# Performance work log

Measured on AMD Instinct MI355X. Metric: run time of the kernel, lower is better.

The kernel has to match this reference:

```python
import jax, jax.numpy as jnp
import numpy as np

B, DIM, DIMH, DIMC = 1024, 32, 1024, 512
SQRT_HALF_PI = float(np.sqrt(np.pi / 2.0))
SQRT2 = float(np.sqrt(2.0))


def _gsp(x):
    """gaussian_softplus activation from ConditionalICNN."""
    return (SQRT_HALF_PI * x * jax.scipy.special.erf(x / SQRT2)
            + jnp.exp(-0.5 * x * x) + SQRT_HALF_PI * x) / (2.0 * SQRT_HALF_PI)


def setup_inputs() -> dict:
    key = jax.random.key(0)
    _i = [0]
    def nrm(shape, s=0.05):
        _i[0] += 1
        return jax.random.normal(jax.random.fold_in(key, _i[0]), shape, dtype=jnp.float32) * s
    inp = {
        "x": nrm((B, DIM), 1.0),
        "c": nrm((B, DIMC), 1.0),
        # w0 init: log(exp(1)-1) as in DeepConvexFlow
        "w0": jnp.full((1,), float(np.log(np.e - 1.0)), dtype=jnp.float32),
        "w1": jnp.zeros((1,), dtype=jnp.float32),
        "Wz0_w": nrm((DIMH, DIM)), "Wz0_b": nrm((DIMH,)),
        "Wc0_w": nrm((DIMH, DIMC)), "Wc0_b": nrm((DIMH,)),
        "an0_b": nrm((DIMH,)), "an0_logs": nrm((DIMH,), 0.01),
        "Wz1_w": nrm((DIMH, DIMH)), "Wz1_b": nrm((DIMH,)),
        "Wx1_w": nrm((DIMH, DIM)), "Wx1_b": nrm((DIMH,)),
        "Wc1_w": nrm((DIMH, DIMC)), "Wc1_b": nrm((DIMH,)),
        "an1_b": nrm((DIMH,)), "an1_logs": nrm((DIMH,), 0.01),
        "Wz2_w": nrm((DIMH, DIMH)), "Wz2_b": nrm((DIMH,)),
        "Wx2_w": nrm((DIMH, DIM)), "Wx2_b": nrm((DIMH,)),
        "Wc2_w": nrm((DIMH, DIMC)), "Wc2_b": nrm((DIMH,)),
        "an2_b": nrm((DIMH,)), "an2_logs": nrm((DIMH,), 0.01),
        "Wzout_w": nrm((1, DIMH)), "Wxout_w": nrm((1, DIM)), "Wcout_w": nrm((1, DIMC)),
    }
    return inp


def reference(x, c, w0, w1,
              Wz0_w, Wz0_b, Wc0_w, Wc0_b, an0_b, an0_logs,
              Wz1_w, Wz1_b, Wx1_w, Wx1_b, Wc1_w, Wc1_b, an1_b, an1_logs,
              Wz2_w, Wz2_b, Wx2_w, Wx2_b, Wc2_w, Wc2_b, an2_b, an2_logs,
              Wzout_w, Wxout_w, Wcout_w):
    """ConditionalDeepConvexFlow.forward_transform with exact logdet.
    Returns (f = grad_x F(x), logdet = logabsdet of per-sample Hessian)."""

    def pot(x1, c1):  # scalar convex potential F for one sample
        h = Wz0_w @ x1 + Wz0_b + Wc0_w @ c1 + Wc0_b
        z = _gsp((h + an0_b) * jnp.exp(an0_logs))  # ActNormNoLogdet + act
        for (Wz_w, Wz_b, Wx_w, Wx_b, Wc_w, Wc_b, an_b, an_logs) in (
                (Wz1_w, Wz1_b, Wx1_w, Wx1_b, Wc1_w, Wc1_b, an1_b, an1_logs),
                (Wz2_w, Wz2_b, Wx2_w, Wx2_b, Wc2_w, Wc2_b, an2_b, an2_logs)):
            # PosLinear: softplus(W) with gain 1/in_features
            h = (jax.nn.softplus(Wz_w) @ z) / DIMH + Wz_b \
                + Wx_w @ x1 + Wx_b + Wc_w @ c1 + Wc_b
            z = _gsp((h + an_b) * jnp.exp(an_logs))
        icnn = (jax.nn.softplus(Wzout_w) @ z)[0] / DIMH \
               + (Wxout_w @ x1)[0] + (Wcout_w @ c1)[0]
        return jax.nn.softplus(w1)[0] * icnn \
               + jax.nn.softplus(w0)[0] * 0.5 * jnp.sum(x1 * x1)

    f = jax.vmap(jax.grad(pot))(x, c)          # [B, DIM]
    H = jax.vmap(jax.hessian(pot))(x, c)       # [B, DIM, DIM]
    logdet = jnp.linalg.slogdet(H)[1]          # [B]
    return f, logdet
```

## Files before the change

### kernel.cpp

```cpp
#include <hip/hip_runtime.h>

constexpr int NB   = 1024;
constexpr int NDIM = 32;
constexpr int NH   = 1024;
constexpr int NC   = 512;
constexpr int NS   = 8;
constexpr int KSF  = 8;

constexpr float INV_SQRT2PI = 0.3989422804014327f;
constexpr float SQRT_HALF   = 0.70710678118654752f;
constexpr float SQRT_HPI    = 1.2533141373155003f;

typedef __attribute__((ext_vector_type(8))) short short8;
typedef __attribute__((ext_vector_type(4))) short short4v;
typedef __attribute__((ext_vector_type(4))) float float4v;

__device__ __forceinline__ float sp_f(float x) {
  return (x > 20.f) ? x : log1pf(expf(x));
}

__device__ __forceinline__ short f2bf(float f) {
  union { float f; unsigned u; } x; x.f = f;
  const unsigned r = x.u + 0x7fffu + ((x.u >> 16) & 1u);
  return (short)(r >> 16);
}

__device__ __forceinline__ float bf2f(short s) {
  union { unsigned u; float f; } c;
  c.u = ((unsigned)(unsigned short)s) << 16;
  return c.f;
}

__device__ __forceinline__ void async_ld16(const void* g, void* l) {
  __builtin_amdgcn_global_load_lds(
      (const __attribute__((address_space(1))) void*)g,
      (__attribute__((address_space(3))) void*)l, 16, 0, 0);
}

__global__ __launch_bounds__(256) void k_prep(
    const float* __restrict__ Wz1, const float* __restrict__ Wz2,
    const float* __restrict__ Wzout, const float* __restrict__ Wz0,
    const float* __restrict__ Wx1, const float* __restrict__ Wx2,
    const float* __restrict__ Wc0, const float* __restrict__ Wc1,
    const float* __restrict__ Wc2, const float* __restrict__ Cc,
    short* __restrict__ S1b, short* __restrict__ S1Tb,
    short* __restrict__ S2b, short* __restrict__ S2Tb,
    short* __restrict__ Wc0b, short* __restrict__ Wc1b, short* __restrict__ Wc2b,
    short* __restrict__ Ccb, short* __restrict__ W0Tb,
    short* __restrict__ Wx1Tb, short* __restrict__ Wx2Tb,
    float* __restrict__ so)
{
  const int idx = blockIdx.x * 256 + threadIdx.x;
  const int i = idx >> 10, p = idx & 1023;
  const float v1 = sp_f(Wz1[idx]);
  const short b1 = f2bf(v1);
  S1b[idx] = b1; S1Tb[p * NH + i] = b1;
  const float v2 = sp_f(Wz2[idx]);
  const short b2 = f2bf(v2);
  S2b[idx] = b2; S2Tb[p * NH + i] = b2;
  if (idx < NH) so[idx] = sp_f(Wzout[idx]);
  if (idx < NH * NC) {
    Wc0b[idx] = f2bf(Wc0[idx]);
    Wc1b[idx] = f2bf(Wc1[idx]);
    Wc2b[idx] = f2bf(Wc2[idx]);
  }
  if (idx < NB * NC) Ccb[idx] = f2bf(Cc[idx]);
  if (idx < NDIM * NH) {
    const int j = idx >> 10, pp = idx & 1023;
    W0Tb[idx]  = f2bf(Wz0[pp * NDIM + j]);
    Wx1Tb[idx] = f2bf(Wx1[pp * NDIM + j]);
    Wx2Tb[idx] = f2bf(Wx2[pp * NDIM + j]);
  }
}

template<int EPI>
__global__ __launch_bounds__(256) void k_gemm(
    const float* __restrict__ A, const float* __restrict__ Bt,
    float* __restrict__ C, int K, int lda, float scale)
{
  __shared__ float As[16][68];
  __shared__ float Bs[16][68];
  const int tid  = threadIdx.y * 16 + threadIdx.x;
  const int arow = tid >> 2;
  const int acol = (tid & 3) << 2;
  const int m0 = blockIdx.y << 6;
  const int n0 = blockIdx.x << 6;

  float acc[4][4];
#pragma unroll
  for (int i = 0; i < 4; ++i)
#pragma unroll
    for (int j = 0; j < 4; ++j) acc[i][j] = 0.f;

  const int R = m0 + arow;
  for (int k0 = 0; k0 < K; k0 += 16) {
    const float4 av = *reinterpret_cast<const float4*>(&A[(size_t)R * lda + k0 + acol]);
    As[acol + 0][arow] = av.x; As[acol + 1][arow] = av.y;
    As[acol + 2][arow] = av.z; As[acol + 3][arow] = av.w;
    const float4 bv = *reinterpret_cast<const float4*>(&Bt[(size_t)(n0 + arow) * K + k0 + acol]);
    Bs[acol + 0][arow] = bv.x; Bs[acol + 1][arow] = bv.y;
    Bs[acol + 2][arow] = bv.z; Bs[acol + 3][arow] = bv.w;
    __syncthreads();
#pragma unroll
    for (int kk = 0; kk < 16; ++kk) {
      const float4 a  = *reinterpret_cast<const float4*>(&As[kk][threadIdx.y << 2]);
      const float4 bb = *reinterpret_cast<const float4*>(&Bs[kk][threadIdx.x << 2]);
      const float am[4] = {a.x, a.y, a.z, a.w};
      const float bn[4] = {bb.x, bb.y, bb.z, bb.w};
#pragma unroll
      for (int i2 = 0; i2 < 4; ++i2)
#pragma unroll
        for (int j2 = 0; j2 < 4; ++j2)
          acc[i2][j2] = fmaf(am[i2], bn[j2], acc[i2][j2]);
    }
    __syncthreads();
  }
#pragma unroll
  for (int i2 = 0; i2 < 4; ++i2) {
    const int row = m0 + (threadIdx.y << 2) + i2;
    const int col = n0 + (threadIdx.x << 2);
    float* cp = &C[(size_t)row * NH + col];
    float4 o;
    o.x = acc[i2][0] * scale; o.y = acc[i2][1] * scale;
    o.z = acc[i2][2] * scale; o.w = acc[i2][3] * scale;
    if constexpr (EPI == 1) {
      const float4 cur = *reinterpret_cast<const float4*>(cp);
      o.x += cur.x; o.y += cur.y; o.z += cur.z; o.w += cur.w;
    }
    *reinterpret_cast<float4*>(cp) = o;
  }
}

__global__ __launch_bounds__(256) void k_m128(
    const short* __restrict__ A, const short* __restrict__ Bt,
    float* __restrict__ C, float scale, int K, int ldc)
{
  __shared__ short As[128 * 32];
  __shared__ short Bs[128 * 32];
  const int tid  = threadIdx.x;
  const int wave = tid >> 6, lane = tid & 63;
  const int m0 = blockIdx.x << 7, n0 = blockIdx.y << 7;
  const int wm = (wave >> 1) << 6, wn = (wave & 1) << 6;
  const int qd = lane >> 4, md = lane & 15;
  const int sr = lane >> 2;
  const int sc = (lane & 3) << 3;

  float4v acc[4][4];
#pragma unroll
  for (int i = 0; i < 4; ++i)
#pragma unroll
    for (int j = 0; j < 4; ++j) acc[i][j] = (float4v)(0.f);

  for (int k0 = 0; k0 < K; k0 += 32) {
#pragma unroll
    for (int i = 0; i < 2; ++i) {
      const int ch  = wave * 2 + i;
      const int row = ch * 16 + sr;
      async_ld16(&A [(size_t)(m0 + row) * K + k0 + sc], &As[ch * 512]);
      async_ld16(&Bt[(size_t)(n0 + row) * K + k0 + sc], &Bs[ch * 512]);
    }
    __syncthreads();
    short8 af[4], bfr[4];
#pragma unroll
    for (int t = 0; t < 4; ++t) {
      af[t]  = *(const short8*)&As[(wm + t * 16 + md) * 32 + qd * 8];
      bfr[t] = *(const short8*)&Bs[(wn + t * 16 + md) * 32 + qd * 8];
    }
#pragma unroll
    for (int i = 0; i < 4; ++i)
#pragma unroll
      for (int j = 0; j < 4; ++j)
        acc[i][j] = __builtin_amdgcn_mfma_f32_16x16x32_bf16(bfr[j], af[i], acc[i][j], 0, 0, 0);
    __syncthreads();
  }

#pragma unroll
  for (int i = 0; i < 4; ++i) {
    const int rowg = m0 + wm + i * 16 + md;
#pragma unroll
    for (int j = 0; j < 4; ++j) {
      const int colb = n0 + wn + j * 16 + (qd << 2);
      float4 o;
      o.x = acc[i][j][0] * scale; o.y = acc[i][j][1] * scale;
      o.z = acc[i][j][2] * scale; o.w = acc[i][j][3] * scale;
      *reinterpret_cast<float4*>(&C[(size_t)rowg * ldc + colb]) = o;
    }
  }
}

template<int EPI>
__global__ __launch_bounds__(256) void k_mgemm(
    const short* __restrict__ A, const short* __restrict__ Bt,
    short* __restrict__ o1, short* __restrict__ o2,
    const float* __restrict__ gvec, const float* __restrict__ dvec,
    const short* __restrict__ wepiT,
    float scale, int K, int b0)
{
  __shared__ short As[128 * 32];
  __shared__ short Bs[128 * 32];
  const int tid  = threadIdx.x;
  const int wave = tid >> 6, lane = tid & 63;
  const int m0 = blockIdx.x << 7, n0 = blockIdx.y << 7;
  const int wm = (wave >> 1) << 6, wn = (wave & 1) << 6;
  const int qd = lane >> 4, md = lane & 15;

  float4v acc[4][4];
#pragma unroll
  for (int i = 0; i < 4; ++i)
#pragma unroll
    for (int j = 0; j < 4; ++j) acc[i][j] = (float4v)(0.f);

  const int sr = lane >> 2;
  const int sc = (lane & 3) << 3;

  for (int k0 = 0; k0 < K; k0 += 32) {
#pragma unroll
    for (int i = 0; i < 2; ++i) {
      const int ch  = wave * 2 + i;
      const int row = ch * 16 + sr;
      async_ld16(&A [(size_t)(m0 + row) * K + k0 + sc], &As[ch * 512]);
      async_ld16(&Bt[(size_t)(n0 + row) * K + k0 + sc], &Bs[ch * 512]);
    }
    __syncthreads();
    short8 af[4], bfr[4];
#pragma unroll
    for (int t = 0; t < 4; ++t) {
      af[t]  = *(const short8*)&As[(wm + t * 16 + md) * 32 + qd * 8];
      bfr[t] = *(const short8*)&Bs[(wn + t * 16 + md) * 32 + qd * 8];
    }
#pragma unroll
    for (int i = 0; i < 4; ++i)
#pragma unroll
      for (int j = 0; j < 4; ++j)
        acc[i][j] = __builtin_amdgcn_mfma_f32_16x16x32_bf16(bfr[j], af[i], acc[i][j], 0, 0, 0);
    __syncthreads();
  }

#pragma unroll
  for (int i = 0; i < 4; ++i) {
    const int rowg = m0 + wm + i * 16 + md;
    const int b = b0 + (rowg >> 5);
    const int j2 = rowg & 31;
    const size_t bNH = (size_t)b * NH;
#pragma unroll
    for (int j = 0; j < 4; ++j) {
      const int colb = n0 + wn + j * 16 + (qd << 2);
      const float4 dq = *(const float4*)&dvec[bNH + colb];
      const short4v wq = *(const short4v*)&wepiT[(size_t)j2 * NH + colb];
      const float dqv[4] = {dq.x, dq.y, dq.z, dq.w};
      float v[4];
      short4v o1v;
#pragma unroll
      for (int r = 0; r < 4; ++r) {
        v[r] = acc[i][j][r] * scale + bf2f(wq[r]);
        o1v[r] = f2bf(v[r] * dqv[r]);
      }
      *(short4v*)&o1[(size_t)rowg * NH + colb] = o1v;
      if constexpr (EPI == 2) {
        const float4 gg = *(const float4*)&gvec[bNH + colb];
        const float ggv[4] = {gg.x, gg.y, gg.z, gg.w};
        short4v o2v;
#pragma unroll
        for (int r = 0; r < 4; ++r) o2v[r] = f2bf(v[r] * ggv[r]);
        *(short4v*)&o2[(size_t)rowg * NH + colb] = o2v;
      }
    }
  }
}

__global__ __launch_bounds__(256) void k_mgemm64(
    const short* __restrict__ A, const short* __restrict__ Bt,
    float* __restrict__ C, float scale, int K)
{
  __shared__ short As[64 * 32];
  __shared__ short Bs[64 * 32];
  const int tid  = threadIdx.x;
  const int wave = tid >> 6, lane = tid & 63;
  const int m0 = blockIdx.x << 6, n0 = blockIdx.y << 6;
  const int wm = (wave >> 1) << 5, wn = (wave & 1) << 5;
  const int qd = lane >> 4, md = lane & 15;
  const int sr = lane >> 2;
  const int sc = (lane & 3) << 3;

  float4v acc[2][2];
#pragma unroll
  for (int i = 0; i < 2; ++i)
#pragma unroll
    for (int j = 0; j < 2; ++j) acc[i][j] = (float4v)(0.f);

  for (int k0 = 0; k0 < K; k0 += 32) {
    const int row = wave * 16 + sr;
    async_ld16(&A [(size_t)(m0 + row) * K + k0 + sc], &As[wave * 512]);
    async_ld16(&Bt[(size_t)(n0 + row) * K + k0 + sc], &Bs[wave * 512]);
    __syncthreads();
    short8 af[2], bfr[2];
#pragma unroll
    for (int t = 0; t < 2; ++t) {
      af[t]  = *(const short8*)&As[(wm + t * 16 + md) * 32 + qd * 8];
      bfr[t] = *(const short8*)&Bs[(wn + t * 16 + md) * 32 + qd * 8];
    }
#pragma unroll
    for (int i = 0; i < 2; ++i)
#pragma unroll
      for (int j = 0; j < 2; ++j)
        acc[i][j] = __builtin_amdgcn_mfma_f32_16x16x32_bf16(bfr[j], af[i], acc[i][j], 0, 0, 0);
    __syncthreads();
  }

#pragma unroll
  for (int i = 0; i < 2; ++i) {
    const int rowg = m0 + wm + i * 16 + md;
#pragma unroll
    for (int j = 0; j < 2; ++j) {
      const int colb = n0 + wn + j * 16 + (qd << 2);
      float4 o;
      o.x = acc[i][j][0] * scale; o.y = acc[i][j][1] * scale;
      o.z = acc[i][j][2] * scale; o.w = acc[i][j][3] * scale;
      *reinterpret_cast<float4*>(&C[(size_t)rowg * NH + colb]) = o;
    }
  }
}

__global__ __launch_bounds__(256) void k_act(
    const float* __restrict__ HP, const float* __restrict__ HPC_l,
    const float* __restrict__ bA, const float* __restrict__ bB,
    const float* __restrict__ bC,
    const float* __restrict__ anb, const float* __restrict__ anl,
    short* __restrict__ Zbf, float* __restrict__ G, float* __restrict__ U,
    int hasC)
{
  const int idx = blockIdx.x * 256 + threadIdx.x;
  const int i = idx & 1023;
  float bias = bA[i] + bB[i] + anb[i];
  if (hasC) bias += bC[i];
  const float el = expf(anl[i]);
  const float hc = HPC_l[(size_t)(idx >> 10) * (3 * NH) + i];
  const float a = (HP[idx] + hc + bias) * el;
  const float pdf = expf(-0.5f * a * a);
  const float er = erff(a * SQRT_HALF);
  Zbf[idx] = f2bf((SQRT_HPI * a * er + pdf + SQRT_HPI * a) * INV_SQRT2PI);
  G[idx] = 0.5f * (1.f + er) * el;
  U[idx] = pdf * INV_SQRT2PI * el * el;
}

__global__ __launch_bounds__(256) void k_act2(
    const float* __restrict__ HP, const float* __restrict__ HPC_l,
    const float* __restrict__ bA, const float* __restrict__ bB,
    const float* __restrict__ bC,
    const float* __restrict__ anb, const float* __restrict__ anl,
    const float* __restrict__ so,
    float* __restrict__ SD2, short* __restrict__ D2gbf)
{
  const int idx = blockIdx.x * 256 + threadIdx.x;
  const int i = idx & 1023;
  const float bias = bA[i] + bB[i] + bC[i] + anb[i];
  const float el = expf(anl[i]);
  const float hc = HPC_l[(size_t)(idx >> 10) * (3 * NH) + i];
  const float a = (HP[idx] + hc + bias) * el;
  const float pdf = expf(-0.5f * a * a);
  const float er = erff(a * SQRT_HALF);
  const float g = 0.5f * (1.f + er) * el;
  const float u = pdf * INV_SQRT2PI * el * el;
  const float t2 = so[i] * (1.f / NH);
  SD2[idx] = sqrtf(fmaxf(t2 * u, 0.f));
  D2gbf[idx] = f2bf(t2 * g);
}

__global__ __launch_bounds__(256) void k_bw1(
    const float* __restrict__ T1, const float* __restrict__ G1,
    const float* __restrict__ U1,
    short* __restrict__ E1bf, float* __restrict__ SD1)
{
  const int idx = blockIdx.x * 256 + threadIdx.x;
  const float t = T1[idx];
  E1bf[idx] = f2bf(t * G1[idx]);
  SD1[idx] = sqrtf(fmaxf(t * U1[idx], 0.f));
}

__global__ __launch_bounds__(256) void k_bw0(
    const float* __restrict__ T0, const float* __restrict__ U0,
    const float* __restrict__ G0,
    float* __restrict__ D0, short* __restrict__ GT0b)
{
  const int idx = blockIdx.x * 256 + threadIdx.x;
  const float t = T0[idx];
  D0[idx] = t * U0[idx];
  GT0b[idx] = f2bf(t * G0[idx]);
}

__global__ __launch_bounds__(256) void k_scale0(
    const float* __restrict__ G0, const float* __restrict__ Wz0,
    short* __restrict__ Ah1, int b0)
{
  const int idx = blockIdx.x * 256 + threadIdx.x;
  const int p = idx & 1023, r = idx >> 10;
  const int b = b0 + (r >> 5), j = r & 31;
  Ah1[idx] = f2bf(G0[(size_t)b * NH + p] * Wz0[p * NDIM + j]);
}

__global__ __launch_bounds__(256) void k_fgemm(
    const short* __restrict__ A0, const short* __restrict__ A1,
    const short* __restrict__ A2,
    const short* __restrict__ W0T, const short* __restrict__ W1T,
    const short* __restrict__ W2T,
    float* __restrict__ partF)
{
  const int mb = blockIdx.x;
  const int ks = blockIdx.y;
  const int term = blockIdx.z;
  const short* A  = (term == 0) ? A0 : (term == 1) ? A1 : A2;
  const short* WT = (term == 0) ? W0T : (term == 1) ? W1T : W2T;
  const int wave = threadIdx.x >> 6, lane = threadIdx.x & 63;
  const int qd = lane >> 4, md = lane & 15;
  const int m0 = mb * 128 + wave * 32;
  const int kbeg = ks * (NH / KSF);

  float4v acc[2][2];
#pragma unroll
  for (int i = 0; i < 2; ++i)
#pragma unroll
    for (int j = 0; j < 2; ++j) acc[i][j] = (float4v)(0.f);

  for (int k0 = kbeg; k0 < kbeg + NH / KSF; k0 += 32) {
    const int kk = k0 + qd * 8;
    short8 af[2], bfr[2];
    af[0]  = *(const short8*)&A[(size_t)(m0 + md) * NH + kk];
    af[1]  = *(const short8*)&A[(size_t)(m0 + 16 + md) * NH + kk];
    bfr[0] = *(const short8*)&WT[(size_t)md * NH + kk];
    bfr[1] = *(const short8*)&WT[(size_t)(16 + md) * NH + kk];
#pragma unroll
    for (int i = 0; i < 2; ++i)
#pragma unroll
      for (int j = 0; j < 2; ++j)
        acc[i][j] = __builtin_amdgcn_mfma_f32_16x16x32_bf16(af[i], bfr[j], acc[i][j], 0, 0, 0);
  }

  float* out = &partF[(size_t)(term * KSF + ks) * NB * 32];
#pragma unroll
  for (int i = 0; i < 2; ++i)
#pragma unroll
    for (int j = 0; j < 2; ++j)
#pragma unroll
      for (int r = 0; r < 4; ++r) {
        const int row = m0 + i * 16 + qd * 4 + r;
        const int col = j * 16 + md;
        out[(size_t)row * 32 + col] = acc[i][j][r];
      }
}

__global__ __launch_bounds__(256) void k_fred(
    const float* __restrict__ partF, const float* __restrict__ X,
    const float* __restrict__ Wxout,
    const float* __restrict__ w0p, const float* __restrict__ w1p,
    float* __restrict__ outF)
{
  const int e = blockIdx.x * 256 + threadIdx.x;
  float s = 0.f;
#pragma unroll
  for (int p = 0; p < 3 * KSF; ++p) s += partF[(size_t)p * NB * 32 + e];
  const float spw0 = sp_f(w0p[0]);
  const float spw1 = sp_f(w1p[0]);
  outF[e] = spw1 * (s + Wxout[e & 31]) + spw0 * X[e];
}

__global__ __launch_bounds__(256) void k_gram(
    const short* __restrict__ Q1, const short* __restrict__ Q2,
    const short* __restrict__ W0T, const float* __restrict__ D0,
    float* __restrict__ partH, int b0)
{
  const int ns = blockIdx.x, bl = blockIdx.y;
  const int b = b0 + bl;
  const int wave = threadIdx.x >> 6, lane = threadIdx.x & 63;
  const int wm = (wave >> 1) << 4, wn = (wave & 1) << 4;
  const int qd = lane >> 4, md = lane & 15;
  const int kbeg = ns << 7;
  const size_t rb = (size_t)bl * 32 * NH;

  float4v acc = (float4v)(0.f);

  for (int k0 = kbeg; k0 < kbeg + 128; k0 += 32) {
    const int kk = k0 + qd * 8;
    const short8 ar = *(const short8*)&W0T[(size_t)(wm + md) * NH + kk];
    float dd[8];
    *(float4*)&dd[0] = *(const float4*)&D0[(size_t)b * NH + kk];
    *(float4*)&dd[4] = *(const float4*)&D0[(size_t)b * NH + kk + 4];
    short8 af;
#pragma unroll
    for (int e = 0; e < 8; ++e) af[e] = f2bf(bf2f(ar[e]) * dd[e]);
    const short8 bfr = *(const short8*)&W0T[(size_t)(wn + md) * NH + kk];
    acc = __builtin_amdgcn_mfma_f32_16x16x32_bf16(af, bfr, acc, 0, 0, 0);
  }
#pragma unroll
  for (int l = 0; l < 2; ++l) {
    const short* Q = (l == 0) ? Q1 : Q2;
    for (int k0 = kbeg; k0 < kbeg + 128; k0 += 32) {
      const int kk = k0 + qd * 8;
      const short8 af  = *(const short8*)&Q[rb + (size_t)(wm + md) * NH + kk];
      const short8 bfr = *(const short8*)&Q[rb + (size_t)(wn + md) * NH + kk];
      acc = __builtin_amdgcn_mfma_f32_16x16x32_bf16(af, bfr, acc, 0, 0, 0);
    }
  }

  float* out = &partH[((size_t)bl * NS + ns) * 1024];
#pragma unroll
  for (int r = 0; r < 4; ++r)
    out[(wm + qd * 4 + r) * 32 + (wn + md)] = acc[r];
}

__global__ __launch_bounds__(256) void k_gram2(
    const float* __restrict__ partH,
    const float* __restrict__ w0p, const float* __restrict__ w1p,
    float* __restrict__ outLD, int b0)
{
  const int bl = blockIdx.x, b = b0 + bl, tid = threadIdx.x;
  __shared__ float sH[32][33];
  __shared__ float sred[32];
  const float spw0 = sp_f(w0p[0]);
  const float spw1 = sp_f(w1p[0]);
  const float* base = &partH[(size_t)bl * NS * 1024];
#pragma unroll
  for (int r = 0; r < 4; ++r) {
    const int e = r * 256 + tid;
    float s = 0.f;
#pragma unroll
    for (int ns = 0; ns < NS; ++ns) s += base[ns * 1024 + e];
    float h = s * spw1;
    const int row = e >> 5, col = e & 31;
    if (row == col) h += spw0;
    sH[row][col] = h;
  }
  __syncthreads();

  float ldacc = 0.f;
  for (int c = 0; c < 32; ++c) {
    if (tid >= c && tid < 32) {
      float s = sH[tid][c];
      for (int m = 0; m < c; ++m) s -= sH[tid][m] * sH[c][m];
      sred[tid] = s;
    }
    __syncthreads();
    const float sc = sred[c];
    if (tid >= c && tid < 32) {
      const float lcc = sqrtf(sc);
      sH[tid][c] = (tid == c) ? lcc : sred[tid] / lcc;
    }
    ldacc += logf(sc);
    __syncthreads();
  }
  if (tid == 0) outLD[b] = ldacc;
}

extern "C" void kernel_launch(void* const* d_in, const int* in_sizes, int n_in,
                              void* d_out, int out_size, void* d_ws, size_t ws_size,
                              hipStream_t stream)
{
  const float* X    = (const float*)d_in[0];
  const float* Cc   = (const float*)d_in[1];
  const float* w0   = (const float*)d_in[2];
  const float* w1   = (const float*)d_in[3];
  const float* Wz0w = (const float*)d_in[4];
  const float* Wz0b = (const float*)d_in[5];
  const float* Wc0w = (const float*)d_in[6];
  const float* Wc0b = (const float*)d_in[7];
  const float* an0b = (const float*)d_in[8];
  const float* an0l = (const float*)d_in[9];
  const float* Wz1w = (const float*)d_in[10];
  const float* Wz1b = (const float*)d_in[11];
  const float* Wx1w = (const float*)d_in[12];
  const float* Wx1b = (const float*)d_in[13];
  const float* Wc1w = (const float*)d_in[14];
  const float* Wc1b = (const float*)d_in[15];
  const float* an1b = (const float*)d_in[16];
  const float* an1l = (const float*)d_in[17];
  const float* Wz2w = (const float*)d_in[18];
  const float* Wz2b = (const float*)d_in[19];
  const float* Wx2w = (const float*)d_in[20];
  const float* Wx2b = (const float*)d_in[21];
  const float* Wc2w = (const float*)d_in[22];
  const float* Wc2b = (const float*)d_in[23];
  const float* an2b = (const float*)d_in[24];
  const float* an2l = (const float*)d_in[25];
  const float* Wzoutw = (const float*)d_in[26];
  const float* Wxoutw = (const float*)d_in[27];

  float* ws = (float*)d_ws;
  size_t off = 0;
  auto alloc = [&](size_t n) {
    float* p = ws + off; off += (n + 3) & ~(size_t)3; return p;
  };
  const size_t HH = (size_t)NH * NH;
  const size_t BH = (size_t)NB * NH;

  short* S1b  = (short*)alloc(HH / 2);
  short* S2b  = (short*)alloc(HH / 2);
  short* S1Tb = (short*)alloc(HH / 2);
  short* S2Tb = (short*)alloc(HH / 2);
  short* Wc0bb = (short*)alloc((size_t)NH * NC / 2);
  short* Wc1bb = (short*)alloc((size_t)NH * NC / 2);
  short* Wc2bb = (short*)alloc((size_t)NH * NC / 2);
  short* Ccb  = (short*)alloc((size_t)NB * NC / 2);
  short* W0Tb = (short*)alloc((size_t)NDIM * NH / 2);
  short* Wx1Tb = (short*)alloc((size_t)NDIM * NH / 2);
  short* Wx2Tb = (short*)alloc((size_t)NDIM * NH / 2);
  float* so   = alloc(NH);
  float* HP   = alloc(BH);
  float* HPC  = alloc((size_t)NB * 3 * NH);
  short* Z0b  = (short*)alloc(BH / 2);
  short* Z1b  = (short*)alloc(BH / 2);
  float* G0   = alloc(BH);
  float* U0   = alloc(BH);
  float* G1   = alloc(BH);
  float* U1   = alloc(BH);
  float* SD2  = alloc(BH);
  short* D2gb = (short*)alloc(BH / 2);
  float* T1   = alloc(BH);
  short* E1b  = (short*)alloc(BH / 2);
  float* SD1  = alloc(BH);
  float* T0   = alloc(BH);
  float* D0   = alloc(BH);
  short* GT0b = (short*)alloc(BH / 2);
  float* partF = alloc((size_t)3 * KSF * NB * 32);

  const size_t avail_f = ws_size / sizeof(float);
  int CB = 32;
  const int cands[6] = {1024, 512, 256, 128, 64, 32};
  for (int ci = 0; ci < 6; ++ci) {
    const size_t need = off + 4 * ((size_t)cands[ci] * 32 * NH / 2 + 4)
                      + (size_t)cands[ci] * NS * 1024 + 64;
    if (need <= avail_f) { CB = cands[ci]; break; }
  }
  const size_t chunk_sh = (size_t)CB * 32 * NH;
  short* Ah1 = (short*)alloc(chunk_sh / 2);
  short* A2b = (short*)alloc(chunk_sh / 2);
  short* Q1b = (short*)alloc(chunk_sh / 2);
  short* Q2b = (short*)alloc(chunk_sh / 2);
  float* partH = alloc((size_t)CB * NS * 1024);

  float* outF  = (float*)d_out;
  float* outLD = (float*)d_out + NB * NDIM;

  const dim3 blk2(16, 16);
  const dim3 gridX(16, NB / 64);
  const dim3 gridE(NB * NH / 256);
  const dim3 grid64(NB / 64, NH / 64);
  const dim3 gridC(NB / 128, 3 * NH / 128);
  const float invH = 1.0f / (float)NH;

  k_prep<<<dim3(HH / 256), dim3(256), 0, stream>>>(
      Wz1w, Wz2w, Wzoutw, Wz0w, Wx1w, Wx2w, Wc0w, Wc1w, Wc2w, Cc,
      S1b, S1Tb, S2b, S2Tb, Wc0bb, Wc1bb, Wc2bb, Ccb, W0Tb, Wx1Tb, Wx2Tb, so);

  k_m128<<<gridC, dim3(256), 0, stream>>>(Ccb, Wc0bb, HPC, 1.f, NC, 3 * NH);

  k_gemm<0><<<gridX, blk2, 0, stream>>>(X, Wz0w, HP, NDIM, NDIM, 1.f);
  k_act<<<gridE, dim3(256), 0, stream>>>(HP, HPC + 0 * NH, Wz0b, Wc0b, nullptr,
                                         an0b, an0l, Z0b, G0, U0, 0);
  k_mgemm64<<<grid64, dim3(256), 0, stream>>>(Z0b, S1b, HP, invH, NH);
  k_gemm<1><<<gridX, blk2, 0, stream>>>(X, Wx1w, HP, NDIM, NDIM, 1.f);
  k_act<<<gridE, dim3(256), 0, stream>>>(HP, HPC + 1 * NH, Wz1b, Wx1b, Wc1b,
                                         an1b, an1l, Z1b, G1, U1, 1);
  k_mgemm64<<<grid64, dim3(256), 0, stream>>>(Z1b, S2b, HP, invH, NH);
  k_gemm<1><<<gridX, blk2, 0, stream>>>(X, Wx2w, HP, NDIM, NDIM, 1.f);
  k_act2<<<gridE, dim3(256), 0, stream>>>(HP, HPC + 2 * NH, Wz2b, Wx2b, Wc2b,
                                          an2b, an2l, so, SD2, D2gb);
  k_mgemm64<<<grid64, dim3(256), 0, stream>>>(D2gb, S2Tb, T1, invH, NH);
  k_bw1<<<gridE, dim3(256), 0, stream>>>(T1, G1, U1, E1b, SD1);
  k_mgemm64<<<grid64, dim3(256), 0, stream>>>(E1b, S1Tb, T0, invH, NH);
  k_bw0<<<gridE, dim3(256), 0, stream>>>(T0, U0, G0, D0, GT0b);

  k_fgemm<<<dim3(8, KSF, 3), dim3(256), 0, stream>>>(
      GT0b, E1b, D2gb, W0Tb, Wx1Tb, Wx2Tb, partF);
  k_fred<<<dim3(NB * 32 / 256), dim3(256), 0, stream>>>(
      partF, X, Wxoutw, w0, w1, outF);

  const dim3 gridJ(CB * 32 / 128, NH / 128);
  const dim3 gridS((size_t)CB * 32 * NH / 256);
  const dim3 gridG(NS, CB);
  for (int b0 = 0; b0 < NB; b0 += CB) {
    k_scale0<<<gridS, dim3(256), 0, stream>>>(G0, Wz0w, Ah1, b0);
    k_mgemm<2><<<gridJ, dim3(256), 0, stream>>>(Ah1, S1b, Q1b, A2b,
                                                G1, SD1, Wx1Tb, invH, NH, b0);
    k_mgemm<1><<<gridJ, dim3(256), 0, stream>>>(A2b, S2b, Q2b, nullptr,
                                                nullptr, SD2, Wx2Tb, invH, NH, b0);
    k_gram<<<gridG, dim3(256), 0, stream>>>(Q1b, Q2b, W0Tb, D0, partH, b0);
    k_gram2<<<dim3(CB), dim3(256), 0, stream>>>(partH, w0, w1, outLD, b0);
  }
}
```

Measured before the change: 756.1 us.

## Batch x-projection GEMMs, split-K the hidden GEMMs, shrink Jacobian GEMM tile

The three small x-projection GEMMs become one launch with a z-dimension, and each adds into the matching slice of the precomputed conditional term. The 1024x1024 hidden GEMMs are split-K into two partial buffers, and the following activation and backward kernels sum and scale them. This doubles the grid and gives more parallelism. The chunked Jacobian GEMM uses 128x64 tiles for more blocks, preloads its epilogue vectors, and reuses the Ah1 buffer for Q2b, which frees workspace for larger chunk sizes. The cost is extra global traffic for the split-K partials.

```diff
diff --git a/kernel.cpp b/kernel.cpp
--- a/kernel.cpp
+++ b/kernel.cpp
@@ -73,11 +73,15 @@
   }
 }
 
-template<int EPI>
-__global__ __launch_bounds__(256) void k_gemm(
-    const float* __restrict__ A, const float* __restrict__ Bt,
-    float* __restrict__ C, int K, int lda, float scale)
-{
+__global__ __launch_bounds__(256) void k_gemmx(
+    const float* __restrict__ A,
+    const float* __restrict__ B0, const float* __restrict__ B1,
+    const float* __restrict__ B2,
+    float* __restrict__ C0, float* __restrict__ C1, float* __restrict__ C2,
+    int ldc)
+{
+  const float* Bt = (blockIdx.z == 0) ? B0 : (blockIdx.z == 1) ? B1 : B2;
+  float* C        = (blockIdx.z == 0) ? C0 : (blockIdx.z == 1) ? C1 : C2;
   __shared__ float As[16][68];
   __shared__ float Bs[16][68];
   const int tid  = threadIdx.y * 16 + threadIdx.x;
@@ -93,11 +97,11 @@
     for (int j = 0; j < 4; ++j) acc[i][j] = 0.f;
 
   const int R = m0 + arow;
-  for (int k0 = 0; k0 < K; k0 += 16) {
-    const float4 av = *reinterpret_cast<const float4*>(&A[(size_t)R * lda + k0 + acol]);
+  for (int k0 = 0; k0 < NDIM; k0 += 16) {
+    const float4 av = *reinterpret_cast<const float4*>(&A[(size_t)R * NDIM + k0 + acol]);
     As[acol + 0][arow] = av.x; As[acol + 1][arow] = av.y;
     As[acol + 2][arow] = av.z; As[acol + 3][arow] = av.w;
-    const float4 bv = *reinterpret_cast<const float4*>(&Bt[(size_t)(n0 + arow) * K + k0 + acol]);
+    const float4 bv = *reinterpret_cast<const float4*>(&Bt[(size_t)(n0 + arow) * NDIM + k0 + acol]);
     Bs[acol + 0][arow] = bv.x; Bs[acol + 1][arow] = bv.y;
     Bs[acol + 2][arow] = bv.z; Bs[acol + 3][arow] = bv.w;
     __syncthreads();
@@ -119,14 +123,11 @@
   for (int i2 = 0; i2 < 4; ++i2) {
     const int row = m0 + (threadIdx.y << 2) + i2;
     const int col = n0 + (threadIdx.x << 2);
-    float* cp = &C[(size_t)row * NH + col];
+    float* cp = &C[(size_t)row * ldc + col];
+    const float4 cur = *reinterpret_cast<const float4*>(cp);
     float4 o;
-    o.x = acc[i2][0] * scale; o.y = acc[i2][1] * scale;
-    o.z = acc[i2][2] * scale; o.w = acc[i2][3] * scale;
-    if constexpr (EPI == 1) {
-      const float4 cur = *reinterpret_cast<const float4*>(cp);
-      o.x += cur.x; o.y += cur.y; o.z += cur.z; o.w += cur.w;
-    }
+    o.x = acc[i2][0] + cur.x; o.y = acc[i2][1] + cur.y;
+    o.z = acc[i2][2] + cur.z; o.w = acc[i2][3] + cur.w;
     *reinterpret_cast<float4*>(cp) = o;
   }
 }
@@ -197,56 +198,70 @@
     float scale, int K, int b0)
 {
   __shared__ short As[128 * 32];
-  __shared__ short Bs[128 * 32];
+  __shared__ short Bs[64 * 32];
   const int tid  = threadIdx.x;
   const int wave = tid >> 6, lane = tid & 63;
-  const int m0 = blockIdx.x << 7, n0 = blockIdx.y << 7;
-  const int wm = (wave >> 1) << 6, wn = (wave & 1) << 6;
+  const int m0 = blockIdx.x << 7, n0 = blockIdx.y << 6;
+  const int wm = (wave >> 1) << 6, wn = (wave & 1) << 5;
   const int qd = lane >> 4, md = lane & 15;
-
-  float4v acc[4][4];
-#pragma unroll
-  for (int i = 0; i < 4; ++i)
-#pragma unroll
-    for (int j = 0; j < 4; ++j) acc[i][j] = (float4v)(0.f);
-
   const int sr = lane >> 2;
   const int sc = (lane & 3) << 3;
 
+  float4v acc[4][2];
+#pragma unroll
+  for (int i = 0; i < 4; ++i)
+#pragma unroll
+    for (int j = 0; j < 2; ++j) acc[i][j] = (float4v)(0.f);
+
   for (int k0 = 0; k0 < K; k0 += 32) {
 #pragma unroll
-    for (int i = 0; i < 2; ++i) {
-      const int ch  = wave * 2 + i;
-      const int row = ch * 16 + sr;
-      async_ld16(&A [(size_t)(m0 + row) * K + k0 + sc], &As[ch * 512]);
-      async_ld16(&Bt[(size_t)(n0 + row) * K + k0 + sc], &Bs[ch * 512]);
-    }
-    __syncthreads();
-    short8 af[4], bfr[4];
-#pragma unroll
-    for (int t = 0; t < 4; ++t) {
+    for (int i = 0; i < 3; ++i) {
+      const int ch = wave * 3 + i;
+      if (ch < 8) {
+        async_ld16(&A[(size_t)(m0 + ch * 16 + sr) * K + k0 + sc], &As[ch * 512]);
+      } else {
+        const int c2 = ch - 8;
+        async_ld16(&Bt[(size_t)(n0 + c2 * 16 + sr) * K + k0 + sc], &Bs[c2 * 512]);
+      }
+    }
+    __syncthreads();
+    short8 af[4], bfr[2];
+#pragma unroll
+    for (int t = 0; t < 4; ++t)
       af[t]  = *(const short8*)&As[(wm + t * 16 + md) * 32 + qd * 8];
+#pragma unroll
+    for (int t = 0; t < 2; ++t)
       bfr[t] = *(const short8*)&Bs[(wn + t * 16 + md) * 32 + qd * 8];
-    }
 #pragma unroll
     for (int i = 0; i < 4; ++i)
 #pragma unroll
-      for (int j = 0; j < 4; ++j)
+      for (int j = 0; j < 2; ++j)
         acc[i][j] = __builtin_amdgcn_mfma_f32_16x16x32_bf16(bfr[j], af[i], acc[i][j], 0, 0, 0);
     __syncthreads();
   }
 
+  const int bbase = b0 + ((m0 + wm) >> 5);
+  const size_t bNH0 = (size_t)bbase * NH, bNH1 = bNH0 + NH;
+  float4 dqA[2], dqB[2], ggA[2], ggB[2];
+#pragma unroll
+  for (int j = 0; j < 2; ++j) {
+    const int colb = n0 + wn + j * 16 + (qd << 2);
+    dqA[j] = *(const float4*)&dvec[bNH0 + colb];
+    dqB[j] = *(const float4*)&dvec[bNH1 + colb];
+    if constexpr (EPI == 2) {
+      ggA[j] = *(const float4*)&gvec[bNH0 + colb];
+      ggB[j] = *(const float4*)&gvec[bNH1 + colb];
+    }
+  }
 #pragma unroll
   for (int i = 0; i < 4; ++i) {
     const int rowg = m0 + wm + i * 16 + md;
-    const int b = b0 + (rowg >> 5);
     const int j2 = rowg & 31;
-    const size_t bNH = (size_t)b * NH;
-#pragma unroll
-    for (int j = 0; j < 4; ++j) {
+#pragma unroll
+    for (int j = 0; j < 2; ++j) {
       const int colb = n0 + wn + j * 16 + (qd << 2);
-      const float4 dq = *(const float4*)&dvec[bNH + colb];
       const short4v wq = *(const short4v*)&wepiT[(size_t)j2 * NH + colb];
+      const float4 dq = (i < 2) ? dqA[j] : dqB[j];
       const float dqv[4] = {dq.x, dq.y, dq.z, dq.w};
       float v[4];
       short4v o1v;
@@ -257,7 +272,7 @@
       }
       *(short4v*)&o1[(size_t)rowg * NH + colb] = o1v;
       if constexpr (EPI == 2) {
-        const float4 gg = *(const float4*)&gvec[bNH + colb];
+        const float4 gg = (i < 2) ? ggA[j] : ggB[j];
         const float ggv[4] = {gg.x, gg.y, gg.z, gg.w};
         short4v o2v;
 #pragma unroll
@@ -270,13 +285,14 @@
 
 __global__ __launch_bounds__(256) void k_mgemm64(
     const short* __restrict__ A, const short* __restrict__ Bt,
-    float* __restrict__ C, float scale, int K)
+    float* __restrict__ Cpart)
 {
   __shared__ short As[64 * 32];
   __shared__ short Bs[64 * 32];
   const int tid  = threadIdx.x;
   const int wave = tid >> 6, lane = tid & 63;
   const int m0 = blockIdx.x << 6, n0 = blockIdx.y << 6;
+  const int kb = blockIdx.z << 9;
   const int wm = (wave >> 1) << 5, wn = (wave & 1) << 5;
   const int qd = lane >> 4, md = lane & 15;
   const int sr = lane >> 2;
@@ -288,10 +304,10 @@
 #pragma unroll
     for (int j = 0; j < 2; ++j) acc[i][j] = (float4v)(0.f);
 
-  for (int k0 = 0; k0 < K; k0 += 32) {
+  for (int k0 = kb; k0 < kb + 512; k0 += 32) {
     const int row = wave * 16 + sr;
-    async_ld16(&A [(size_t)(m0 + row) * K + k0 + sc], &As[wave * 512]);
-    async_ld16(&Bt[(size_t)(n0 + row) * K + k0 + sc], &Bs[wave * 512]);
+    async_ld16(&A [(size_t)(m0 + row) * NH + k0 + sc], &As[wave * 512]);
+    async_ld16(&Bt[(size_t)(n0 + row) * NH + k0 + sc], &Bs[wave * 512]);
     __syncthreads();
     short8 af[2], bfr[2];
 #pragma unroll
@@ -307,6 +323,7 @@
     __syncthreads();
   }
 
+  float* out = Cpart + (size_t)blockIdx.z * NB * NH;
 #pragma unroll
   for (int i = 0; i < 2; ++i) {
     const int rowg = m0 + wm + i * 16 + md;
@@ -314,20 +331,20 @@
     for (int j = 0; j < 2; ++j) {
       const int colb = n0 + wn + j * 16 + (qd << 2);
       float4 o;
-      o.x = acc[i][j][0] * scale; o.y = acc[i][j][1] * scale;
-      o.z = acc[i][j][2] * scale; o.w = acc[i][j][3] * scale;
-      *reinterpret_cast<float4*>(&C[(size_t)rowg * NH + colb]) = o;
+      o.x = acc[i][j][0]; o.y = acc[i][j][1];
+      o.z = acc[i][j][2]; o.w = acc[i][j][3];
+      *reinterpret_cast<float4*>(&out[(size_t)rowg * NH + colb]) = o;
     }
   }
 }
 
 __global__ __launch_bounds__(256) void k_act(
-    const float* __restrict__ HP, const float* __restrict__ HPC_l,
+    const float* __restrict__ HP2, const float* __restrict__ HPC_l,
     const float* __restrict__ bA, const float* __restrict__ bB,
     const float* __restrict__ bC,
     const float* __restrict__ anb, const float* __restrict__ anl,
     short* __restrict__ Zbf, float* __restrict__ G, float* __restrict__ U,
-    int hasC)
+    int hasC, float scale)
 {
   const int idx = blockIdx.x * 256 + threadIdx.x;
   const int i = idx & 1023;
@@ -335,7 +352,8 @@
   if (hasC) bias += bC[i];
   const float el = expf(anl[i]);
   const float hc = HPC_l[(size_t)(idx >> 10) * (3 * NH) + i];
-  const float a = (HP[idx] + hc + bias) * el;
+  const float hp = HP2 ? (HP2[idx] + HP2[(size_t)NB * NH + idx]) * scale : 0.f;
+  const float a = (hp + hc + bias) * el;
   const float pdf = expf(-0.5f * a * a);
   const float er = erff(a * SQRT_HALF);
   Zbf[idx] = f2bf((SQRT_HPI * a * er + pdf + SQRT_HPI * a) * INV_SQRT2PI);
@@ -344,19 +362,20 @@
 }
 
 __global__ __launch_bounds__(256) void k_act2(
-    const float* __restrict__ HP, const float* __restrict__ HPC_l,
+    const float* __restrict__ HP2, const float* __restrict__ HPC_l,
     const float* __restrict__ bA, const float* __restrict__ bB,
     const float* __restrict__ bC,
     const float* __restrict__ anb, const float* __restrict__ anl,
     const float* __restrict__ so,
-    float* __restrict__ SD2, short* __restrict__ D2gbf)
+    float* __restrict__ SD2, short* __restrict__ D2gbf, float scale)
 {
   const int idx = blockIdx.x * 256 + threadIdx.x;
   const int i = idx & 1023;
   const float bias = bA[i] + bB[i] + bC[i] + anb[i];
   const float el = expf(anl[i]);
   const float hc = HPC_l[(size_t)(idx >> 10) * (3 * NH) + i];
-  const float a = (HP[idx] + hc + bias) * el;
+  const float hp = (HP2[idx] + HP2[(size_t)NB * NH + idx]) * scale;
+  const float a = (hp + hc + bias) * el;
   const float pdf = expf(-0.5f * a * a);
   const float er = erff(a * SQRT_HALF);
   const float g = 0.5f * (1.f + er) * el;
@@ -367,23 +386,23 @@
 }
 
 __global__ __launch_bounds__(256) void k_bw1(
-    const float* __restrict__ T1, const float* __restrict__ G1,
+    const float* __restrict__ T2, const float* __restrict__ G1,
     const float* __restrict__ U1,
-    short* __restrict__ E1bf, float* __restrict__ SD1)
+    short* __restrict__ E1bf, float* __restrict__ SD1, float scale)
 {
   const int idx = blockIdx.x * 256 + threadIdx.x;
-  const float t = T1[idx];
+  const float t = (T2[idx] + T2[(size_t)NB * NH + idx]) * scale;
   E1bf[idx] = f2bf(t * G1[idx]);
   SD1[idx] = sqrtf(fmaxf(t * U1[idx], 0.f));
 }
 
 __global__ __launch_bounds__(256) void k_bw0(
-    const float* __restrict__ T0, const float* __restrict__ U0,
+    const float* __restrict__ T2, const float* __restrict__ U0,
     const float* __restrict__ G0,
-    float* __restrict__ D0, short* __restrict__ GT0b)
+    float* __restrict__ D0, short* __restrict__ GT0b, float scale)
 {
   const int idx = blockIdx.x * 256 + threadIdx.x;
-  const float t = T0[idx];
+  const float t = (T2[idx] + T2[(size_t)NB * NH + idx]) * scale;
   D0[idx] = t * U0[idx];
   GT0b[idx] = f2bf(t * G0[idx]);
 }
@@ -603,7 +622,7 @@
   short* Wx1Tb = (short*)alloc((size_t)NDIM * NH / 2);
   short* Wx2Tb = (short*)alloc((size_t)NDIM * NH / 2);
   float* so   = alloc(NH);
-  float* HP   = alloc(BH);
+  float* HP2  = alloc(2 * BH);
   float* HPC  = alloc((size_t)NB * 3 * NH);
   short* Z0b  = (short*)alloc(BH / 2);
   short* Z1b  = (short*)alloc(BH / 2);
@@ -613,10 +632,8 @@
   float* U1   = alloc(BH);
   float* SD2  = alloc(BH);
   short* D2gb = (short*)alloc(BH / 2);
-  float* T1   = alloc(BH);
   short* E1b  = (short*)alloc(BH / 2);
   float* SD1  = alloc(BH);
-  float* T0   = alloc(BH);
   float* D0   = alloc(BH);
   short* GT0b = (short*)alloc(BH / 2);
   float* partF = alloc((size_t)3 * KSF * NB * 32);
@@ -625,7 +642,7 @@
   int CB = 32;
   const int cands[6] = {1024, 512, 256, 128, 64, 32};
   for (int ci = 0; ci < 6; ++ci) {
-    const size_t need = off + 4 * ((size_t)cands[ci] * 32 * NH / 2 + 4)
+    const size_t need = off + 3 * ((size_t)cands[ci] * 32 * NH / 2 + 4)
                       + (size_t)cands[ci] * NS * 1024 + 64;
     if (need <= avail_f) { CB = cands[ci]; break; }
   }
@@ -633,16 +650,16 @@
   short* Ah1 = (short*)alloc(chunk_sh / 2);
   short* A2b = (short*)alloc(chunk_sh / 2);
   short* Q1b = (short*)alloc(chunk_sh / 2);
-  short* Q2b = (short*)alloc(chunk_sh / 2);
+  short* Q2b = Ah1;
   float* partH = alloc((size_t)CB * NS * 1024);
 
   float* outF  = (float*)d_out;
   float* outLD = (float*)d_out + NB * NDIM;
 
   const dim3 blk2(16, 16);
-  const dim3 gridX(16, NB / 64);
+  const dim3 gridXz(16, NB / 64, 3);
   const dim3 gridE(NB * NH / 256);
-  const dim3 grid64(NB / 64, NH / 64);
+  const dim3 grid64(NB / 64, NH / 64, 2);
   const dim3 gridC(NB / 128, 3 * NH / 128);
   const float invH = 1.0f / (float)NH;
 
@@ -651,29 +668,28 @@
       S1b, S1Tb, S2b, S2Tb, Wc0bb, Wc1bb, Wc2bb, Ccb, W0Tb, Wx1Tb, Wx2Tb, so);
 
   k_m128<<<gridC, dim3(256), 0, stream>>>(Ccb, Wc0bb, HPC, 1.f, NC, 3 * NH);
-
-  k_gemm<0><<<gridX, blk2, 0, stream>>>(X, Wz0w, HP, NDIM, NDIM, 1.f);
-  k_act<<<gridE, dim3(256), 0, stream>>>(HP, HPC + 0 * NH, Wz0b, Wc0b, nullptr,
-                                         an0b, an0l, Z0b, G0, U0, 0);
-  k_mgemm64<<<grid64, dim3(256), 0, stream>>>(Z0b, S1b, HP, invH, NH);
-  k_gemm<1><<<gridX, blk2, 0, stream>>>(X, Wx1w, HP, NDIM, NDIM, 1.f);
-  k_act<<<gridE, dim3(256), 0, stream>>>(HP, HPC + 1 * NH, Wz1b, Wx1b, Wc1b,
-                                         an1b, an1l, Z1b, G1, U1, 1);
-  k_mgemm64<<<grid64, dim3(256), 0, stream>>>(Z1b, S2b, HP, invH, NH);
-  k_gemm<1><<<gridX, blk2, 0, stream>>>(X, Wx2w, HP, NDIM, NDIM, 1.f);
-  k_act2<<<gridE, dim3(256), 0, stream>>>(HP, HPC + 2 * NH, Wz2b, Wx2b, Wc2b,
-                                          an2b, an2l, so, SD2, D2gb);
-  k_mgemm64<<<grid64, dim3(256), 0, stream>>>(D2gb, S2Tb, T1, invH, NH);
-  k_bw1<<<gridE, dim3(256), 0, stream>>>(T1, G1, U1, E1b, SD1);
-  k_mgemm64<<<grid64, dim3(256), 0, stream>>>(E1b, S1Tb, T0, invH, NH);
-  k_bw0<<<gridE, dim3(256), 0, stream>>>(T0, U0, G0, D0, GT0b);
+  k_gemmx<<<gridXz, blk2, 0, stream>>>(X, Wz0w, Wx1w, Wx2w,
+                                       HPC + 0 * NH, HPC + 1 * NH, HPC + 2 * NH, 3 * NH);
+
+  k_act<<<gridE, dim3(256), 0, stream>>>(nullptr, HPC + 0 * NH, Wz0b, Wc0b, nullptr,
+                                         an0b, an0l, Z0b, G0, U0, 0, 0.f);
+  k_mgemm64<<<grid64, dim3(256), 0, stream>>>(Z0b, S1b, HP2);
+  k_act<<<gridE, dim3(256), 0, stream>>>(HP2, HPC + 1 * NH, Wz1b, Wx1b, Wc1b,
+                                         an1b, an1l, Z1b, G1, U1, 1, invH);
+  k_mgemm64<<<grid64, dim3(256), 0, stream>>>(Z1b, S2b, HP2);
+  k_act2<<<gridE, dim3(256), 0, stream>>>(HP2, HPC + 2 * NH, Wz2b, Wx2b, Wc2b,
+                                          an2b, an2l, so, SD2, D2gb, invH);
+  k_mgemm64<<<grid64, dim3(256), 0, stream>>>(D2gb, S2Tb, HP2);
+  k_bw1<<<gridE, dim3(256), 0, stream>>>(HP2, G1, U1, E1b, SD1, invH);
+  k_mgemm64<<<grid64, dim3(256), 0, stream>>>(E1b, S1Tb, HP2);
+  k_bw0<<<gridE, dim3(256), 0, stream>>>(HP2, U0, G0, D0, GT0b, invH);
 
   k_fgemm<<<dim3(8, KSF, 3), dim3(256), 0, stream>>>(
       GT0b, E1b, D2gb, W0Tb, Wx1Tb, Wx2Tb, partF);
   k_fred<<<dim3(NB * 32 / 256), dim3(256), 0, stream>>>(
       partF, X, Wxoutw, w0, w1, outF);
 
-  const dim3 gridJ(CB * 32 / 128, NH / 128);
+  const dim3 gridJ(CB * 32 / 128, NH / 64);
   const dim3 gridS((size_t)CB * 32 * NH / 256);
   const dim3 gridG(NS, CB);
   for (int b0 = 0; b0 < NB; b0 += CB) {
```

New measurement: 721.7 us. -4.5%, faster.
